# Kernel tuning notes

Hardware: AMD Instinct MI355X
Metric: run time of the kernel (lower is better)

## Reference

```python
import jax, jax.numpy as jnp
import numpy as np

L, D, H, HID, V, MAXLEN = 4, 768, 12, 3072, 32000, 1024
HD = D // H

def _pe_table(max_len, d_model):
    pos = np.arange(max_len)[:, None].astype(np.float64)
    i = np.arange(d_model)[None, :]
    ang = pos / np.power(10000.0, 2 * (i // 2) / d_model)
    ang[:, 0::2] = np.sin(ang[:, 0::2])
    ang[:, 1::2] = np.cos(ang[:, 1::2])
    return jnp.asarray(ang, dtype=jnp.float32)

def _layernorm(x, g, b, eps=1e-5):
    mu = jnp.mean(x, axis=-1, keepdims=True)
    var = jnp.mean(jnp.square(x - mu), axis=-1, keepdims=True)
    return (x - mu) * jax.lax.rsqrt(var + eps) * g + b

def setup_inputs() -> dict:
    key = jax.random.key(0)
    ks = jax.random.split(key, 16)
    s = 0.02
    inp = {
        'tokens': jax.random.randint(ks[0], (4, 1024), 0, V),
        'emb': jax.random.normal(ks[1], (V, D), jnp.float32) * s,
        'pe': _pe_table(MAXLEN, D),
        'ln1_g': jnp.ones((L, D), jnp.float32), 'ln1_b': jnp.zeros((L, D), jnp.float32),
        'wq': jax.random.normal(ks[2], (L, D, D), jnp.float32) * s, 'bq': jnp.zeros((L, D), jnp.float32),
        'wk': jax.random.normal(ks[3], (L, D, D), jnp.float32) * s, 'bk': jnp.zeros((L, D), jnp.float32),
        'wv': jax.random.normal(ks[4], (L, D, D), jnp.float32) * s, 'bv': jnp.zeros((L, D), jnp.float32),
        'wo': jax.random.normal(ks[5], (L, D, D), jnp.float32) * s, 'bo': jnp.zeros((L, D), jnp.float32),
        'ln2_g': jnp.ones((L, D), jnp.float32), 'ln2_b': jnp.zeros((L, D), jnp.float32),
        'w1': jax.random.normal(ks[6], (L, D, HID), jnp.float32) * s, 'b1': jnp.zeros((L, HID), jnp.float32),
        'w2': jax.random.normal(ks[7], (L, HID, D), jnp.float32) * s, 'b2': jnp.zeros((L, D), jnp.float32),
        'lnf_g': jnp.ones((D,), jnp.float32), 'lnf_b': jnp.zeros((D,), jnp.float32),
        'w_out': jax.random.normal(ks[8], (D, V), jnp.float32) * s,
    }
    return inp

def reference(tokens, emb, pe, ln1_g, ln1_b, wq, bq, wk, bk, wv, bv, wo, bo, ln2_g, ln2_b, w1, b1, w2, b2, lnf_g, lnf_b, w_out):
    B, S = tokens.shape
    x = emb[tokens] + pe[:S]  # [B,S,D]
    causal = jnp.tril(jnp.ones((S, S), bool))  # True = keep
    scale = 1.0 / jnp.sqrt(jnp.float32(D))  # NOTE: module scales by sqrt(d_model), not sqrt(head_dim)
    for l in range(L):
        h = _layernorm(x, ln1_g[l], ln1_b[l])
        def heads(w, b):
            return (h @ w + b).reshape(B, S, H, HD).transpose(0, 2, 1, 3)  # [B,H,S,HD]
        q, k, v = heads(wq[l], bq[l]), heads(wk[l], bk[l]), heads(wv[l], bv[l])
        scores = jnp.einsum('bhqd,bhkd->bhqk', q, k) * scale
        scores = jnp.where(causal, scores, -jnp.inf)
        probs = jax.nn.softmax(scores, axis=-1)
        attn = jnp.einsum('bhqk,bhkd->bhqd', probs, v)
        attn = attn.transpose(0, 2, 1, 3).reshape(B, S, D)
        x = x + attn @ wo[l] + bo[l]
        h2 = _layernorm(x, ln2_g[l], ln2_b[l])
        x = x + jax.nn.relu(h2 @ w1[l] + b1[l]) @ w2[l] + b2[l]
    hs = _layernorm(x, lnf_g, lnf_b)
    return hs @ w_out  # [B,S,V]
```

## Files before the change

kernel.cpp:

```cpp
#include <hip/hip_runtime.h>


typedef __bf16 bf16_t;
typedef bf16_t bf16x8 __attribute__((ext_vector_type(8)));
typedef bf16_t bf16x4 __attribute__((ext_vector_type(4)));
typedef float f32x4 __attribute__((ext_vector_type(4)));

#define GLD16(G, L) __builtin_amdgcn_global_load_lds(                          \
    (const __attribute__((address_space(1))) unsigned int*)(const void*)(G),   \
    (__attribute__((address_space(3))) unsigned int*)(void*)(L), 16, 0, 0)

__device__ __forceinline__ f32x4 mfma16(bf16x8 a, bf16x8 b, f32x4 c) {
  return __builtin_amdgcn_mfma_f32_16x16x32_bf16(a, b, c, 0, 0, 0);
}

__device__ __forceinline__ void barrier_raw() {
  asm volatile("s_barrier" ::: "memory");
}

#define RED16_MAX(x) { x = fmaxf(x, __shfl_xor(x, 1)); x = fmaxf(x, __shfl_xor(x, 2)); \
                       x = fmaxf(x, __shfl_xor(x, 4)); x = fmaxf(x, __shfl_xor(x, 8)); }
#define RED16_SUM(x) { x += __shfl_xor(x, 1); x += __shfl_xor(x, 2); \
                       x += __shfl_xor(x, 4); x += __shfl_xor(x, 8); }

__device__ __forceinline__ int SW64(int row, int col) {
  return row * 64 + (col ^ ((row & 7) << 3));
}

__global__ __launch_bounds__(256)
void tconv_k(const float* __restrict__ in, bf16_t* __restrict__ out, int K, int N,
             size_t in_ls, size_t out_ls) {
  __shared__ float tile[32][33];
  in  += (size_t)blockIdx.z * in_ls;
  out += (size_t)blockIdx.z * out_ls;
  const int n0 = blockIdx.x * 32, k0 = blockIdx.y * 32;
  const int tx = threadIdx.x & 31, ty = threadIdx.x >> 5;
#pragma unroll
  for (int j = 0; j < 4; ++j)
    tile[ty + j * 8][tx] = in[(size_t)(k0 + ty + j * 8) * N + n0 + tx];
  __syncthreads();
#pragma unroll
  for (int j = 0; j < 4; ++j)
    out[(size_t)(n0 + ty + j * 8) * K + k0 + tx] = (bf16_t)tile[tx][ty + j * 8];
}

__global__ void qkvbias_k(const float* __restrict__ bq, const float* __restrict__ bk,
                          const float* __restrict__ bv, float* __restrict__ out) {
  const int l = blockIdx.x;
  for (int j = threadIdx.x; j < 2304; j += 256) {
    float v = (j < 768) ? bq[l * 768 + j]
            : (j < 1536) ? bk[l * 768 + j - 768]
                         : bv[l * 768 + j - 1536];
    out[l * 2304 + j] = v;
  }
}

__global__ __launch_bounds__(256)
void embed_k(const int* __restrict__ tok, const float* __restrict__ emb,
             const float* __restrict__ pe, float* __restrict__ xf) {
  const int row = blockIdx.x, tid = threadIdx.x;
  const int s = row & 1023;
  const int t = tok[row];
  float* o = xf + (size_t)row * 768;
  const float* e = emb + (size_t)t * 768;
  const float* p = pe + (size_t)s * 768;
  o[tid]       = e[tid]       + p[tid];
  o[tid + 256] = e[tid + 256] + p[tid + 256];
  o[tid + 512] = e[tid + 512] + p[tid + 512];
}

__global__ __launch_bounds__(256)
void ln_k(const float* __restrict__ x, const float* __restrict__ g,
          const float* __restrict__ bb, bf16_t* __restrict__ out) {
  const int wave = threadIdx.x >> 6, lane = threadIdx.x & 63;
  const int row = blockIdx.x * 4 + wave;
  const float* xr = x + (size_t)row * 768;
  f32x4 v[3];
#pragma unroll
  for (int c = 0; c < 3; ++c) v[c] = *(const f32x4*)&xr[c * 256 + lane * 4];
  float s = 0.0f;
#pragma unroll
  for (int c = 0; c < 3; ++c)
#pragma unroll
    for (int i = 0; i < 4; ++i) s += v[c][i];
#pragma unroll
  for (int off = 32; off; off >>= 1) s += __shfl_xor(s, off);
  const float mu = s * (1.0f / 768.0f);
  float s2 = 0.0f;
#pragma unroll
  for (int c = 0; c < 3; ++c)
#pragma unroll
    for (int i = 0; i < 4; ++i) {
      const float d = v[c][i] - mu;
      s2 += d * d;
    }
#pragma unroll
  for (int off = 32; off; off >>= 1) s2 += __shfl_xor(s2, off);
  const float rstd = rsqrtf(s2 * (1.0f / 768.0f) + 1e-5f);
  bf16_t* orow = out + (size_t)row * 768;
#pragma unroll
  for (int c = 0; c < 3; ++c) {
    const f32x4 gv = *(const f32x4*)&g[c * 256 + lane * 4];
    const f32x4 bv = *(const f32x4*)&bb[c * 256 + lane * 4];
    bf16x4 o;
#pragma unroll
    for (int i = 0; i < 4; ++i)
      o[i] = (bf16_t)((v[c][i] - mu) * rstd * gv[i] + bv[i]);
    *(bf16x4*)&orow[c * 256 + lane * 4] = o;
  }
}

template <bool BIAS, bool RELU, bool OUTF32, bool NT, int SUPER>
__global__ __launch_bounds__(512, 2)
void gemm8p(const bf16_t* __restrict__ A, const bf16_t* __restrict__ BT,
            const float* __restrict__ bias,
            float* __restrict__ outF, bf16_t* __restrict__ outB,
            int M, int N, int K) {
  extern __shared__ char smem[];
  const int NT_TILES = K >> 6;
  const int tilesM = M >> 8;
  const int cpx = gridDim.x >> 3;
  const int blk = ((int)blockIdx.x & 7) * cpx + ((int)blockIdx.x >> 3);
  int tm, tn;
  if (SUPER > 0) {
    const int grp = SUPER * tilesM;
    const int g = blk / grp, r = blk % grp;
    tm = r / SUPER;
    tn = g * SUPER + r % SUPER;
  } else {
    tm = blk % tilesM;
    tn = blk / tilesM;
  }
  const int tid = threadIdx.x;
  const int lane = tid & 63, wave = tid >> 6;
  const int wr = wave >> 2, wc = wave & 3;
  const int lrow = lane & 15, koct = lane >> 4;

  const size_t rowK = (size_t)K * 2;
  const int srow = tid >> 3;
  const int cswz = ((tid & 7) ^ (srow & 7)) << 4;
  const char* gA = (const char*)(A + (size_t)tm * 256 * K) + (size_t)srow * rowK + cswz;
  const char* gB = (const char*)(BT + (size_t)tn * 256 * K) + (size_t)srow * rowK + cswz;

  const int swz = (lrow & 7) << 4;
  const int aB0 = (wr * 128 + lrow) * 128 + ((koct * 16) ^ swz);
  const int bB0 = 32768 + (wc * 64 + lrow) * 128 + ((koct * 16) ^ swz);

  auto stageA = [&](int t) {
    char* d = smem + ((t & 1) << 16);
    const size_t kb = (size_t)t * 128;
    GLD16(gA + kb,              d + tid * 16);
    GLD16(gA + 64 * rowK + kb,  d + 8192 + tid * 16);
    GLD16(gA + 128 * rowK + kb, d + 16384 + tid * 16);
    GLD16(gA + 192 * rowK + kb, d + 24576 + tid * 16);
  };
  auto stageB = [&](int t) {
    char* d = smem + ((t & 1) << 16) + 32768;
    const size_t kb = (size_t)t * 128;
    GLD16(gB + kb,              d + tid * 16);
    GLD16(gB + 64 * rowK + kb,  d + 8192 + tid * 16);
    GLD16(gB + 128 * rowK + kb, d + 16384 + tid * 16);
    GLD16(gB + 192 * rowK + kb, d + 24576 + tid * 16);
  };

  stageA(0); stageB(0);
  stageA(1); stageB(1);

  f32x4 acc[8][4] = {};

  for (int t = 0; t < NT_TILES; ++t) {
    const char* rb = smem + ((t & 1) << 16);
    const bool pf = (t + 2) < NT_TILES;
    if (t == NT_TILES - 1) asm volatile("s_waitcnt vmcnt(0)" ::: "memory");
    else                   asm volatile("s_waitcnt vmcnt(8)" ::: "memory");
    barrier_raw();

    bf16x8 a0[4][2], a1[4][2], b[4][2];
#pragma unroll
    for (int mi = 0; mi < 4; ++mi) {
      const int o = aB0 + mi * 2048;
      a0[mi][0] = *(const bf16x8*)(rb + o);
      a0[mi][1] = *(const bf16x8*)(rb + (o ^ 64));
    }
#pragma unroll
    for (int ni = 0; ni < 2; ++ni) {
      const int o = bB0 + ni * 2048;
      b[ni][0] = *(const bf16x8*)(rb + o);
      b[ni][1] = *(const bf16x8*)(rb + (o ^ 64));
    }
    barrier_raw();
    __builtin_amdgcn_s_setprio(1);
#pragma unroll
    for (int mi = 0; mi < 4; ++mi)
#pragma unroll
      for (int ni = 0; ni < 2; ++ni) {
        acc[mi][ni] = mfma16(a0[mi][0], b[ni][0], acc[mi][ni]);
        acc[mi][ni] = mfma16(a0[mi][1], b[ni][1], acc[mi][ni]);
      }
    __builtin_amdgcn_s_setprio(0);
    barrier_raw();

#pragma unroll
    for (int ni = 2; ni < 4; ++ni) {
      const int o = bB0 + ni * 2048;
      b[ni][0] = *(const bf16x8*)(rb + o);
      b[ni][1] = *(const bf16x8*)(rb + (o ^ 64));
    }
    __builtin_amdgcn_s_setprio(1);
#pragma unroll
    for (int mi = 0; mi < 4; ++mi)
#pragma unroll
      for (int ni = 2; ni < 4; ++ni) {
        acc[mi][ni] = mfma16(a0[mi][0], b[ni][0], acc[mi][ni]);
        acc[mi][ni] = mfma16(a0[mi][1], b[ni][1], acc[mi][ni]);
      }
    __builtin_amdgcn_s_setprio(0);
    asm volatile("s_waitcnt lgkmcnt(0)" ::: "memory");
    barrier_raw();

    if (pf) stageB(t + 2);
#pragma unroll
    for (int mi = 0; mi < 4; ++mi) {
      const int o = aB0 + (mi + 4) * 2048;
      a1[mi][0] = *(const bf16x8*)(rb + o);
      a1[mi][1] = *(const bf16x8*)(rb + (o ^ 64));
    }
    __builtin_amdgcn_s_setprio(1);
#pragma unroll
    for (int mi = 0; mi < 4; ++mi)
#pragma unroll
      for (int ni = 0; ni < 2; ++ni) {
        acc[mi + 4][ni] = mfma16(a1[mi][0], b[ni][0], acc[mi + 4][ni]);
        acc[mi + 4][ni] = mfma16(a1[mi][1], b[ni][1], acc[mi + 4][ni]);
      }
    __builtin_amdgcn_s_setprio(0);
    asm volatile("s_waitcnt lgkmcnt(0)" ::: "memory");
    barrier_raw();

    if (pf) stageA(t + 2);
    __builtin_amdgcn_s_setprio(1);
#pragma unroll
    for (int mi = 0; mi < 4; ++mi)
#pragma unroll
      for (int ni = 2; ni < 4; ++ni) {
        acc[mi + 4][ni] = mfma16(a1[mi][0], b[ni][0], acc[mi + 4][ni]);
        acc[mi + 4][ni] = mfma16(a1[mi][1], b[ni][1], acc[mi + 4][ni]);
      }
    __builtin_amdgcn_s_setprio(0);
  }

  barrier_raw();
  const int row0 = tm * 256 + wr * 128, col0 = tn * 256 + wc * 64;
  float bv[4];
#pragma unroll
  for (int ni = 0; ni < 4; ++ni)
    bv[ni] = BIAS ? bias[col0 + ni * 16 + lrow] : 0.0f;

  if (OUTF32) {
    float* lf = (float*)smem + wave * (32 * 68);
#pragma unroll
    for (int ph = 0; ph < 4; ++ph) {
#pragma unroll
      for (int mm = 0; mm < 2; ++mm) {
        const int mi = ph * 2 + mm;
#pragma unroll
        for (int ni = 0; ni < 4; ++ni)
#pragma unroll
          for (int r = 0; r < 4; ++r) {
            float v = acc[mi][ni][r] + bv[ni];
            if (RELU) v = fmaxf(v, 0.0f);
            lf[(mm * 16 + koct * 4 + r) * 68 + ni * 16 + lrow] = v;
          }
      }
#pragma unroll
      for (int j = 0; j < 8; ++j) {
        const int lr = j * 4 + koct;
        const int lc = lrow * 4;
        f32x4 v4 = *(const f32x4*)&lf[lr * 68 + lc];
        f32x4* dst = (f32x4*)&outF[(size_t)(row0 + ph * 32 + lr) * N + col0 + lc];
        if (NT) __builtin_nontemporal_store(v4, dst);
        else    *dst = v4;
      }
    }
  } else {
    bf16_t* lb = (bf16_t*)smem + wave * (32 * 72);
#pragma unroll
    for (int ph = 0; ph < 4; ++ph) {
#pragma unroll
      for (int mm = 0; mm < 2; ++mm) {
        const int mi = ph * 2 + mm;
#pragma unroll
        for (int ni = 0; ni < 4; ++ni)
#pragma unroll
          for (int r = 0; r < 4; ++r) {
            float v = acc[mi][ni][r] + bv[ni];
            if (RELU) v = fmaxf(v, 0.0f);
            lb[(mm * 16 + koct * 4 + r) * 72 + ni * 16 + lrow] = (bf16_t)v;
          }
      }
#pragma unroll
      for (int j = 0; j < 4; ++j) {
        const int lr = j * 8 + (lane >> 3);
        const int lc = (lane & 7) * 8;
        bf16x8 v8 = *(const bf16x8*)&lb[lr * 72 + lc];
        *(bf16x8*)&outB[(size_t)(row0 + ph * 32 + lr) * N + col0 + lc] = v8;
      }
    }
  }
}

template <bool BIAS, bool RELU>
__global__ __launch_bounds__(512, 4)
void gemm128(const bf16_t* __restrict__ A, const bf16_t* __restrict__ BT,
             const float* __restrict__ bias, bf16_t* __restrict__ outB,
             int M, int N, int K) {
  extern __shared__ char smem[];
  const int NT_TILES = K >> 6;
  const int tilesM = M >> 7;
  const int cpx = gridDim.x >> 3;
  const int blk = ((int)blockIdx.x & 7) * cpx + ((int)blockIdx.x >> 3);
  const int tm = blk % tilesM, tn = blk / tilesM;
  const int tid = threadIdx.x;
  const int lane = tid & 63, wave = tid >> 6;
  const int wr = wave >> 2, wc = wave & 3;
  const int lrow = lane & 15, koct = lane >> 4;

  const size_t rowK = (size_t)K * 2;
  const int srow = tid >> 3;
  const int cswz = ((tid & 7) ^ (srow & 7)) << 4;
  const char* gA = (const char*)(A + (size_t)tm * 128 * K) + (size_t)srow * rowK + cswz;
  const char* gB = (const char*)(BT + (size_t)tn * 128 * K) + (size_t)srow * rowK + cswz;

  const int swz = (lrow & 7) << 4;
  const int aB0 = (wr * 64 + lrow) * 128 + ((koct * 16) ^ swz);
  const int bB0 = 16384 + (wc * 32 + lrow) * 128 + ((koct * 16) ^ swz);

  auto stage = [&](int t) {
    char* d = smem + ((t & 1) << 15);
    const size_t kb = (size_t)t * 128;
    GLD16(gA + kb,             d + tid * 16);
    GLD16(gA + 64 * rowK + kb, d + 8192 + tid * 16);
    GLD16(gB + kb,             d + 16384 + tid * 16);
    GLD16(gB + 64 * rowK + kb, d + 24576 + tid * 16);
  };

  stage(0); stage(1);

  f32x4 acc[4][2] = {};

  for (int t = 0; t < NT_TILES; ++t) {
    const char* rb = smem + ((t & 1) << 15);
    const bool pf = (t + 2) < NT_TILES;
    if (t == NT_TILES - 1) asm volatile("s_waitcnt vmcnt(0)" ::: "memory");
    else                   asm volatile("s_waitcnt vmcnt(4)" ::: "memory");
    barrier_raw();

    bf16x8 a[4], b[2], a2[4], b2[2];
#pragma unroll
    for (int mi = 0; mi < 4; ++mi) a[mi] = *(const bf16x8*)(rb + aB0 + mi * 2048);
#pragma unroll
    for (int ni = 0; ni < 2; ++ni) b[ni] = *(const bf16x8*)(rb + bB0 + ni * 2048);
    barrier_raw();
    __builtin_amdgcn_s_setprio(1);
#pragma unroll
    for (int mi = 0; mi < 4; ++mi)
#pragma unroll
      for (int ni = 0; ni < 2; ++ni)
        acc[mi][ni] = mfma16(a[mi], b[ni], acc[mi][ni]);
    __builtin_amdgcn_s_setprio(0);

#pragma unroll
    for (int mi = 0; mi < 4; ++mi) a2[mi] = *(const bf16x8*)(rb + ((aB0 + mi * 2048) ^ 64));
#pragma unroll
    for (int ni = 0; ni < 2; ++ni) b2[ni] = *(const bf16x8*)(rb + ((bB0 + ni * 2048) ^ 64));
    __builtin_amdgcn_s_setprio(1);
#pragma unroll
    for (int mi = 0; mi < 4; ++mi)
#pragma unroll
      for (int ni = 0; ni < 2; ++ni)
        acc[mi][ni] = mfma16(a2[mi], b2[ni], acc[mi][ni]);
    __builtin_amdgcn_s_setprio(0);
    asm volatile("s_waitcnt lgkmcnt(0)" ::: "memory");
    barrier_raw();
    if (pf) stage(t + 2);
  }

  const int row0 = tm * 128 + wr * 64, col0 = tn * 128 + wc * 32;
  bf16_t* lb = (bf16_t*)smem + wave * (64 * 36);
#pragma unroll
  for (int ni = 0; ni < 2; ++ni) {
    const float bv = BIAS ? bias[col0 + ni * 16 + lrow] : 0.0f;
#pragma unroll
    for (int mi = 0; mi < 4; ++mi)
#pragma unroll
      for (int r = 0; r < 4; ++r) {
        float v = acc[mi][ni][r] + bv;
        if (RELU) v = fmaxf(v, 0.0f);
        lb[(mi * 16 + koct * 4 + r) * 36 + ni * 16 + lrow] = (bf16_t)v;
      }
  }
#pragma unroll
  for (int j = 0; j < 4; ++j) {
    const int lr = j * 16 + (lane >> 2);
    const int lc = (lane & 3) * 8;
    bf16x8 v8 = *(const bf16x8*)&lb[lr * 36 + lc];
    *(bf16x8*)&outB[(size_t)(row0 + lr) * N + col0 + lc] = v8;
  }
}

template <bool BIAS, bool RELU, bool RESID, bool OUTF32>
__global__ __launch_bounds__(256, 2)
void gemmS(const bf16_t* __restrict__ A, const bf16_t* __restrict__ BT,
           const float* __restrict__ bias, const float* __restrict__ resid,
           float* __restrict__ outF, bf16_t* __restrict__ outB,
           int M, int N, int K) {
  extern __shared__ char smem[];
  const int NT = K >> 6;
  const int tiles_n = N >> 7;
  const int tm = blockIdx.x / tiles_n, tn = blockIdx.x % tiles_n;
  const int tid = threadIdx.x;
  const int wave = tid >> 6, lane = tid & 63;
  const int wr = wave >> 1, wc = wave & 1;
  const int lrow = lane & 15, koct = lane >> 4;

  const char* gA[2];
  const char* gB[4];
  {
    const char* Ab = (const char*)(A + (size_t)tm * 64 * K);
    const char* Bb = (const char*)(BT + (size_t)tn * 128 * K);
#pragma unroll
    for (int i = 0; i < 2; ++i) {
      const int off = i * 4096 + tid * 16;
      const int row = off >> 7;
      const int src = off ^ ((row & 7) << 4);
      gA[i] = Ab + (size_t)row * (2 * K) + (src & 127);
    }
#pragma unroll
    for (int i = 0; i < 4; ++i) {
      const int off = i * 4096 + tid * 16;
      const int row = off >> 7;
      const int src = off ^ ((row & 7) << 4);
      gB[i] = Bb + (size_t)row * (2 * K) + (src & 127);
    }
  }

  int aoff[2][2], boff[2][4];
#pragma unroll
  for (int kk = 0; kk < 2; ++kk) {
#pragma unroll
    for (int mi = 0; mi < 2; ++mi) {
      const int row = wr * 32 + mi * 16 + lrow;
      aoff[kk][mi] = (row * 128 + kk * 64 + koct * 16) ^ ((lrow & 7) << 4);
    }
#pragma unroll
    for (int ni = 0; ni < 4; ++ni) {
      const int row = wc * 64 + ni * 16 + lrow;
      boff[kk][ni] = 8192 + ((row * 128 + kk * 64 + koct * 16) ^ ((lrow & 7) << 4));
    }
  }

#pragma unroll
  for (int t = 0; t < 2; ++t) {
    char* sb = smem + t * 24576;
    const size_t kb = (size_t)t * 128;
    GLD16(gA[0] + kb, sb + tid * 16);
    GLD16(gA[1] + kb, sb + 4096 + tid * 16);
    GLD16(gB[0] + kb, sb + 8192 + tid * 16);
    GLD16(gB[1] + kb, sb + 12288 + tid * 16);
    GLD16(gB[2] + kb, sb + 16384 + tid * 16);
    GLD16(gB[3] + kb, sb + 20480 + tid * 16);
  }

  f32x4 acc[2][4] = {};

  for (int t = 0; t < NT; ++t) {
    char* sb = smem + (t % 3) * 24576;
    char* sb2 = smem + ((t + 2) % 3) * 24576;
    const bool pf = (t + 2) < NT;
    const size_t kb2 = (size_t)(t + 2) * 128;

    if (t == NT - 1) asm volatile("s_waitcnt vmcnt(0)" ::: "memory");
    else             asm volatile("s_waitcnt vmcnt(6)" ::: "memory");
    barrier_raw();

#pragma unroll
    for (int kk = 0; kk < 2; ++kk) {
      bf16x8 af[2], bfr[4];
#pragma unroll
      for (int mi = 0; mi < 2; ++mi)
        af[mi] = *(const bf16x8*)(sb + aoff[kk][mi]);
#pragma unroll
      for (int ni = 0; ni < 4; ++ni)
        bfr[ni] = *(const bf16x8*)(sb + boff[kk][ni]);
      if (pf) {
        if (kk == 0) {
          GLD16(gA[0] + kb2, sb2 + tid * 16);
          GLD16(gA[1] + kb2, sb2 + 4096 + tid * 16);
          GLD16(gB[0] + kb2, sb2 + 8192 + tid * 16);
        } else {
          GLD16(gB[1] + kb2, sb2 + 12288 + tid * 16);
          GLD16(gB[2] + kb2, sb2 + 16384 + tid * 16);
          GLD16(gB[3] + kb2, sb2 + 20480 + tid * 16);
        }
      }
      barrier_raw();
      __builtin_amdgcn_s_setprio(1);
#pragma unroll
      for (int mi = 0; mi < 2; ++mi)
#pragma unroll
        for (int ni = 0; ni < 4; ++ni)
          acc[mi][ni] = mfma16(af[mi], bfr[ni], acc[mi][ni]);
      __builtin_amdgcn_s_setprio(0);
    }
  }

  const int row0 = tm * 64 + wr * 32, col0 = tn * 128 + wc * 64;
#pragma unroll
  for (int ni = 0; ni < 4; ++ni) {
    const int col = col0 + ni * 16 + lrow;
    const float bv = BIAS ? bias[col] : 0.0f;
#pragma unroll
    for (int mi = 0; mi < 2; ++mi) {
#pragma unroll
      for (int r = 0; r < 4; ++r) {
        const int row = row0 + mi * 16 + koct * 4 + r;
        float v = acc[mi][ni][r] + bv;
        if (RELU) v = fmaxf(v, 0.0f);
        const size_t idx = (size_t)row * N + col;
        if (RESID) v += resid[idx];
        if (OUTF32) outF[idx] = v;
        else        outB[idx] = (bf16_t)v;
      }
    }
  }
}

__global__ __launch_bounds__(256)
void attn_k(const bf16_t* __restrict__ qkv, bf16_t* __restrict__ ab) {
  __shared__ __align__(16) bf16_t Qs[64 * 64];
  __shared__ __align__(16) bf16_t Ks[64 * 64];
  __shared__ __align__(16) bf16_t Vt[64 * 64];
  __shared__ __align__(16) bf16_t Ps[4][16 * 64];
  const int qt = blockIdx.x, h = blockIdx.y, b = blockIdx.z;
  const int tid = threadIdx.x;
  const int wave = tid >> 6, lane = tid & 63;
  const int lrow = lane & 15, koct = lane >> 4;
  const float scale = 0.03608439182435161f;

  const size_t RS = 2304;
  const bf16_t* qbase = qkv + h * 64;
  const bf16_t* kbase = qkv + 768 + h * 64;
  const bf16_t* vbase = qkv + 1536 + h * 64;

  const int sr = tid >> 3;
  const int sc = (((tid & 7) ^ (sr & 7)) << 3);

  {
#pragma unroll
    for (int i = 0; i < 2; ++i)
      GLD16(qbase + (size_t)(b * 1024 + qt * 64 + i * 32 + sr) * RS + sc,
            Qs + i * 2048 + tid * 8);
  }
  __syncthreads();
  bf16x8 qf[2];
  qf[0] = *(const bf16x8*)&Qs[SW64(wave * 16 + lrow, koct * 8)];
  qf[1] = *(const bf16x8*)&Qs[SW64(wave * 16 + lrow, 32 + koct * 8)];

  float m_r[4], l_r[4];
  f32x4 o[4] = {};
#pragma unroll
  for (int r = 0; r < 4; ++r) { m_r[r] = -1e30f; l_r[r] = 0.0f; }

  for (int kt = 0; kt <= qt; ++kt) {
    __syncthreads();
    {
#pragma unroll
      for (int i = 0; i < 2; ++i)
        GLD16(kbase + (size_t)(b * 1024 + kt * 64 + i * 32 + sr) * RS + sc,
              Ks + i * 2048 + tid * 8);
    }
    {
      const int kvr = lane;
      const int d0 = wave * 16;
      const bf16_t* vr = vbase + (size_t)(b * 1024 + kt * 64 + kvr) * RS + d0;
      bf16x8 v0 = *(const bf16x8*)vr;
      bf16x8 v1 = *(const bf16x8*)(vr + 8);
#pragma unroll
      for (int j = 0; j < 8; ++j) {
        Vt[(d0 + j) * 64 + (kvr ^ (j << 3))]     = v0[j];
        Vt[(d0 + 8 + j) * 64 + (kvr ^ (j << 3))] = v1[j];
      }
    }
    __syncthreads();

    f32x4 s[4] = {};
#pragma unroll
    for (int ni = 0; ni < 4; ++ni) {
      bf16x8 kf0 = *(const bf16x8*)&Ks[SW64(ni * 16 + lrow, koct * 8)];
      bf16x8 kf1 = *(const bf16x8*)&Ks[SW64(ni * 16 + lrow, 32 + koct * 8)];
      s[ni] = mfma16(qf[0], kf0, s[ni]);
      s[ni] = mfma16(qf[1], kf1, s[ni]);
    }

    const int qrow = qt * 64 + wave * 16 + koct * 4;
    float rm[4];
#pragma unroll
    for (int r = 0; r < 4; ++r) rm[r] = -1e30f;
#pragma unroll
    for (int ni = 0; ni < 4; ++ni) {
      const int kcol = kt * 64 + ni * 16 + lrow;
#pragma unroll
      for (int r = 0; r < 4; ++r) {
        float v = s[ni][r] * scale;
        if (kcol > qrow + r) v = -1e30f;
        s[ni][r] = v;
        rm[r] = fmaxf(rm[r], v);
      }
    }
#pragma unroll
    for (int r = 0; r < 4; ++r) RED16_MAX(rm[r]);
    float corr[4], ps[4];
#pragma unroll
    for (int r = 0; r < 4; ++r) {
      const float mn = fmaxf(m_r[r], rm[r]);
      corr[r] = __expf(m_r[r] - mn);
      m_r[r] = mn;
      ps[r] = 0.0f;
    }
#pragma unroll
    for (int ni = 0; ni < 4; ++ni)
#pragma unroll
      for (int r = 0; r < 4; ++r) {
        const float p = __expf(s[ni][r] - m_r[r]);
        s[ni][r] = p;
        ps[r] += p;
      }
#pragma unroll
    for (int r = 0; r < 4; ++r) RED16_SUM(ps[r]);
#pragma unroll
    for (int r = 0; r < 4; ++r) l_r[r] = l_r[r] * corr[r] + ps[r];
#pragma unroll
    for (int ni = 0; ni < 4; ++ni)
#pragma unroll
      for (int r = 0; r < 4; ++r) o[ni][r] *= corr[r];

#pragma unroll
    for (int ni = 0; ni < 4; ++ni)
#pragma unroll
      for (int r = 0; r < 4; ++r) {
        const int prow = koct * 4 + r;
        Ps[wave][prow * 64 + ((ni * 16 + lrow) ^ ((prow & 7) << 3))] =
            (bf16_t)s[ni][r];
      }
    __syncthreads();

    bf16x8 pa0 = *(const bf16x8*)&Ps[wave][SW64(lrow, koct * 8)];
    bf16x8 pa1 = *(const bf16x8*)&Ps[wave][SW64(lrow, 32 + koct * 8)];
#pragma unroll
    for (int ni = 0; ni < 4; ++ni) {
      bf16x8 vf0 = *(const bf16x8*)&Vt[SW64(ni * 16 + lrow, koct * 8)];
      bf16x8 vf1 = *(const bf16x8*)&Vt[SW64(ni * 16 + lrow, 32 + koct * 8)];
      o[ni] = mfma16(pa0, vf0, o[ni]);
      o[ni] = mfma16(pa1, vf1, o[ni]);
    }
  }

#pragma unroll
  for (int r = 0; r < 4; ++r) {
    const float inv = 1.0f / l_r[r];
    const int row = qt * 64 + wave * 16 + koct * 4 + r;
#pragma unroll
    for (int ni = 0; ni < 4; ++ni)
      ab[(size_t)(b * 1024 + row) * 768 + h * 64 + ni * 16 + lrow] =
          (bf16_t)(o[ni][r] * inv);
  }
}

extern "C" void kernel_launch(void* const* d_in, const int* in_sizes, int n_in,
                              void* d_out, int out_size, void* d_ws, size_t ws_size,
                              hipStream_t stream) {
  (void)in_sizes; (void)n_in; (void)out_size; (void)ws_size;
  const int*   tok   = (const int*)d_in[0];
  const float* emb   = (const float*)d_in[1];
  const float* pe    = (const float*)d_in[2];
  const float* ln1_g = (const float*)d_in[3];
  const float* ln1_b = (const float*)d_in[4];
  const float* wq    = (const float*)d_in[5];
  const float* bq    = (const float*)d_in[6];
  const float* wk    = (const float*)d_in[7];
  const float* bk    = (const float*)d_in[8];
  const float* wv    = (const float*)d_in[9];
  const float* bv    = (const float*)d_in[10];
  const float* wo    = (const float*)d_in[11];
  const float* bo    = (const float*)d_in[12];
  const float* ln2_g = (const float*)d_in[13];
  const float* ln2_b = (const float*)d_in[14];
  const float* w1    = (const float*)d_in[15];
  const float* b1    = (const float*)d_in[16];
  const float* w2    = (const float*)d_in[17];
  const float* b2    = (const float*)d_in[18];
  const float* lnf_g = (const float*)d_in[19];
  const float* lnf_b = (const float*)d_in[20];
  const float* w_out = (const float*)d_in[21];
  float* out = (float*)d_out;

  char* ws = (char*)d_ws;
  size_t off = 0;
  auto alloc = [&](size_t bytes) -> void* {
    void* p = ws + off;
    off += (bytes + 255) & ~(size_t)255;
    return p;
  };
  float*  xf      = (float*)alloc(4096ull * 768 * 4);
  bf16_t* hb      = (bf16_t*)alloc(4096ull * 768 * 2);
  bf16_t* qkvb    = (bf16_t*)alloc(4096ull * 2304 * 2);
  bf16_t* ab      = (bf16_t*)alloc(4096ull * 768 * 2);
  bf16_t* fb      = (bf16_t*)alloc(4096ull * 3072 * 2);
  float*  qkvbias = (float*)alloc(4ull * 2304 * 4);
  bf16_t* wqkvT   = (bf16_t*)alloc(4ull * 2304 * 768 * 2);
  bf16_t* woT     = (bf16_t*)alloc(4ull * 768 * 768 * 2);
  bf16_t* w1T     = (bf16_t*)alloc(4ull * 3072 * 768 * 2);
  bf16_t* w2T     = (bf16_t*)alloc(4ull * 768 * 3072 * 2);
  bf16_t* woutT   = (bf16_t*)alloc(32000ull * 768 * 2);

  tconv_k<<<dim3(24, 24, 4), 256, 0, stream>>>(wq, wqkvT, 768, 768,
      768ull * 768, 2304ull * 768);
  tconv_k<<<dim3(24, 24, 4), 256, 0, stream>>>(wk, wqkvT + 768ull * 768, 768, 768,
      768ull * 768, 2304ull * 768);
  tconv_k<<<dim3(24, 24, 4), 256, 0, stream>>>(wv, wqkvT + 2ull * 768 * 768, 768, 768,
      768ull * 768, 2304ull * 768);
  tconv_k<<<dim3(24, 24, 4), 256, 0, stream>>>(wo, woT, 768, 768,
      768ull * 768, 768ull * 768);
  tconv_k<<<dim3(96, 24, 4), 256, 0, stream>>>(w1, w1T, 768, 3072,
      768ull * 3072, 3072ull * 768);
  tconv_k<<<dim3(24, 96, 4), 256, 0, stream>>>(w2, w2T, 3072, 768,
      3072ull * 768, 768ull * 3072);
  tconv_k<<<dim3(1000, 24, 1), 256, 0, stream>>>(w_out, woutT, 768, 32000, 0, 0);
  qkvbias_k<<<4, 256, 0, stream>>>(bq, bk, bv, qkvbias);

  embed_k<<<4096, 256, 0, stream>>>(tok, emb, pe, xf);

  const size_t SMEM8P  = 131072;
  const size_t SMEM128 = 65536;
  const size_t SMEMS   = 3 * 24576;
  for (int l = 0; l < 4; ++l) {
    ln_k<<<1024, 256, 0, stream>>>(xf, ln1_g + l * 768, ln1_b + l * 768, hb);
    gemm128<true, false><<<32 * 18, 512, SMEM128, stream>>>(
        hb, wqkvT + (size_t)l * 2304 * 768, qkvbias + l * 2304,
        qkvb, 4096, 2304, 768);
    attn_k<<<dim3(16, 12, 4), 256, 0, stream>>>(qkvb, ab);
    gemmS<true, false, true, true><<<64 * 6, 256, SMEMS, stream>>>(
        ab, woT + (size_t)l * 768 * 768, bo + l * 768,
        xf, xf, nullptr, 4096, 768, 768);
    ln_k<<<1024, 256, 0, stream>>>(xf, ln2_g + l * 768, ln2_b + l * 768, hb);
    gemm128<true, true><<<32 * 24, 512, SMEM128, stream>>>(
        hb, w1T + (size_t)l * 3072 * 768, b1 + l * 3072,
        fb, 4096, 3072, 768);
    gemmS<true, false, true, true><<<64 * 6, 256, SMEMS, stream>>>(
        fb, w2T + (size_t)l * 768 * 3072, b2 + l * 768,
        xf, xf, nullptr, 4096, 768, 3072);
  }
  ln_k<<<1024, 256, 0, stream>>>(xf, lnf_g, lnf_b, hb);
  gemm8p<false, false, true, true, 5><<<16 * 125, 512, SMEM8P, stream>>>(
      hb, woutT, nullptr, out, nullptr, 4096, 32000, 768);
}
```

Measured before the change: 1.048 ms.

## Add 256-thread 128x128 GEMM kernel and rebalance GEMM kernels across layers

Adds a new gemmV kernel: 128x128 tiles, 4 waves each computing a 64x64 sub-tile, BK=32 double-buffered with global_load_lds, 32 KB shared memory and up to 4 blocks per CU. It replaces gemm128 for the FFN up-projection and gemm8p for the vocabulary projection. The QKV projection moves to the large 256-row gemm8p tile. The aim is better occupancy and per-wave register reuse on the largest GEMMs. The trade-off is shorter K steps per barrier, and a different grid size and tail balance per GEMM.

```diff
diff --git a/kernel.cpp b/kernel.cpp
--- a/kernel.cpp
+++ b/kernel.cpp
@@ -107,6 +107,144 @@
     for (int i = 0; i < 4; ++i)
       o[i] = (bf16_t)((v[c][i] - mu) * rstd * gv[i] + bv[i]);
     *(bf16x4*)&orow[c * 256 + lane * 4] = o;
+  }
+}
+
+template <bool BIAS, bool RELU, bool OUTF32, bool NT, int SUPER>
+__global__ __launch_bounds__(256, 4)
+void gemmV(const bf16_t* __restrict__ A, const bf16_t* __restrict__ BT,
+           const float* __restrict__ bias,
+           float* __restrict__ outF, bf16_t* __restrict__ outB,
+           int M, int N, int K) {
+  extern __shared__ char smem[];
+  const int NT_TILES = K >> 5;
+  const int tilesM = M >> 7;
+  const int cpx = gridDim.x >> 3;
+  const int blk = ((int)blockIdx.x & 7) * cpx + ((int)blockIdx.x >> 3);
+  int tm, tn;
+  if (SUPER > 0) {
+    const int grp = SUPER * tilesM;
+    const int g = blk / grp, r = blk % grp;
+    tm = r / SUPER;
+    tn = g * SUPER + r % SUPER;
+  } else {
+    tm = blk % tilesM;
+    tn = blk / tilesM;
+  }
+  const int tid = threadIdx.x;
+  const int lane = tid & 63, wave = tid >> 6;
+  const int wr = wave >> 1, wc = wave & 1;
+  const int lrow = lane & 15, koct = lane >> 4;
+
+  const size_t rowK = (size_t)K * 2;
+  const int srow = tid >> 2;
+  const int cswz = ((tid & 3) ^ ((tid >> 3) & 3)) << 4;
+  const char* gA = (const char*)(A + (size_t)tm * 128 * K) + (size_t)srow * rowK + cswz;
+  const char* gB = (const char*)(BT + (size_t)tn * 128 * K) + (size_t)srow * rowK + cswz;
+
+  const int fkey = (lrow >> 1) & 3;
+  const int aB0 = (wr * 64 + lrow) * 64 + ((koct ^ fkey) << 4);
+  const int bB0 = 8192 + (wc * 64 + lrow) * 64 + ((koct ^ fkey) << 4);
+
+  auto stage = [&](int t) {
+    char* d = smem + ((t & 1) << 14);
+    const size_t kb = (size_t)t * 64;
+    GLD16(gA + kb,             d + tid * 16);
+    GLD16(gA + 64 * rowK + kb, d + 4096 + tid * 16);
+    GLD16(gB + kb,             d + 8192 + tid * 16);
+    GLD16(gB + 64 * rowK + kb, d + 12288 + tid * 16);
+  };
+
+  stage(0); stage(1);
+
+  f32x4 acc[4][4] = {};
+
+  for (int t = 0; t < NT_TILES; ++t) {
+    const char* rb = smem + ((t & 1) << 14);
+    const bool pf = (t + 2) < NT_TILES;
+    if (t == NT_TILES - 1) asm volatile("s_waitcnt vmcnt(0)" ::: "memory");
+    else                   asm volatile("s_waitcnt vmcnt(4)" ::: "memory");
+    barrier_raw();
+
+    bf16x8 a[4], b[4];
+#pragma unroll
+    for (int mi = 0; mi < 4; ++mi) a[mi] = *(const bf16x8*)(rb + aB0 + mi * 1024);
+#pragma unroll
+    for (int ni = 0; ni < 2; ++ni) b[ni] = *(const bf16x8*)(rb + bB0 + ni * 1024);
+    barrier_raw();
+    __builtin_amdgcn_s_setprio(1);
+#pragma unroll
+    for (int mi = 0; mi < 4; ++mi)
+#pragma unroll
+      for (int ni = 0; ni < 2; ++ni)
+        acc[mi][ni] = mfma16(a[mi], b[ni], acc[mi][ni]);
+    __builtin_amdgcn_s_setprio(0);
+
+#pragma unroll
+    for (int ni = 2; ni < 4; ++ni) b[ni] = *(const bf16x8*)(rb + bB0 + ni * 1024);
+    __builtin_amdgcn_s_setprio(1);
+#pragma unroll
+    for (int mi = 0; mi < 4; ++mi)
+#pragma unroll
+      for (int ni = 2; ni < 4; ++ni)
+        acc[mi][ni] = mfma16(a[mi], b[ni], acc[mi][ni]);
+    __builtin_amdgcn_s_setprio(0);
+    asm volatile("s_waitcnt lgkmcnt(0)" ::: "memory");
+    barrier_raw();
+    if (pf) stage(t + 2);
+  }
+
+  const int row0 = tm * 128 + wr * 64, col0 = tn * 128 + wc * 64;
+  float bv[4];
+#pragma unroll
+  for (int ni = 0; ni < 4; ++ni)
+    bv[ni] = BIAS ? bias[col0 + ni * 16 + lrow] : 0.0f;
+
+  if (OUTF32) {
+    float* lf = (float*)(smem + wave * 8192);
+#pragma unroll
+    for (int p = 0; p < 2; ++p) {
+#pragma unroll
+      for (int mm = 0; mm < 2; ++mm) {
+        const int mi = p * 2 + mm;
+#pragma unroll
+        for (int ni = 0; ni < 4; ++ni)
+#pragma unroll
+          for (int r = 0; r < 4; ++r) {
+            float v = acc[mi][ni][r] + bv[ni];
+            if (RELU) v = fmaxf(v, 0.0f);
+            lf[(mm * 16 + koct * 4 + r) * 64 + ni * 16 + lrow] = v;
+          }
+      }
+#pragma unroll
+      for (int j = 0; j < 8; ++j) {
+        const int lr = j * 4 + koct;
+        const int lc = lrow * 4;
+        f32x4 v4 = *(const f32x4*)&lf[lr * 64 + lc];
+        f32x4* dst = (f32x4*)&outF[(size_t)(row0 + p * 32 + lr) * N + col0 + lc];
+        if (NT) __builtin_nontemporal_store(v4, dst);
+        else    *dst = v4;
+      }
+    }
+  } else {
+    bf16_t* lb = (bf16_t*)(smem + wave * 8192);
+#pragma unroll
+    for (int mi = 0; mi < 4; ++mi)
+#pragma unroll
+      for (int ni = 0; ni < 4; ++ni)
+#pragma unroll
+        for (int r = 0; r < 4; ++r) {
+          float v = acc[mi][ni][r] + bv[ni];
+          if (RELU) v = fmaxf(v, 0.0f);
+          lb[(mi * 16 + koct * 4 + r) * 64 + ni * 16 + lrow] = (bf16_t)v;
+        }
+#pragma unroll
+    for (int j = 0; j < 8; ++j) {
+      const int lr = j * 8 + (lane >> 3);
+      const int lc = (lane & 7) * 8;
+      bf16x8 v8 = *(const bf16x8*)&lb[lr * 64 + lc];
+      *(bf16x8*)&outB[(size_t)(row0 + lr) * N + col0 + lc] = v8;
+    }
   }
 }
 
@@ -306,105 +444,6 @@
         *(bf16x8*)&outB[(size_t)(row0 + ph * 32 + lr) * N + col0 + lc] = v8;
       }
     }
-  }
-}
-
-template <bool BIAS, bool RELU>
-__global__ __launch_bounds__(512, 4)
-void gemm128(const bf16_t* __restrict__ A, const bf16_t* __restrict__ BT,
-             const float* __restrict__ bias, bf16_t* __restrict__ outB,
-             int M, int N, int K) {
-  extern __shared__ char smem[];
-  const int NT_TILES = K >> 6;
-  const int tilesM = M >> 7;
-  const int cpx = gridDim.x >> 3;
-  const int blk = ((int)blockIdx.x & 7) * cpx + ((int)blockIdx.x >> 3);
-  const int tm = blk % tilesM, tn = blk / tilesM;
-  const int tid = threadIdx.x;
-  const int lane = tid & 63, wave = tid >> 6;
-  const int wr = wave >> 2, wc = wave & 3;
-  const int lrow = lane & 15, koct = lane >> 4;
-
-  const size_t rowK = (size_t)K * 2;
-  const int srow = tid >> 3;
-  const int cswz = ((tid & 7) ^ (srow & 7)) << 4;
-  const char* gA = (const char*)(A + (size_t)tm * 128 * K) + (size_t)srow * rowK + cswz;
-  const char* gB = (const char*)(BT + (size_t)tn * 128 * K) + (size_t)srow * rowK + cswz;
-
-  const int swz = (lrow & 7) << 4;
-  const int aB0 = (wr * 64 + lrow) * 128 + ((koct * 16) ^ swz);
-  const int bB0 = 16384 + (wc * 32 + lrow) * 128 + ((koct * 16) ^ swz);
-
-  auto stage = [&](int t) {
-    char* d = smem + ((t & 1) << 15);
-    const size_t kb = (size_t)t * 128;
-    GLD16(gA + kb,             d + tid * 16);
-    GLD16(gA + 64 * rowK + kb, d + 8192 + tid * 16);
-    GLD16(gB + kb,             d + 16384 + tid * 16);
-    GLD16(gB + 64 * rowK + kb, d + 24576 + tid * 16);
-  };
-
-  stage(0); stage(1);
-
-  f32x4 acc[4][2] = {};
-
-  for (int t = 0; t < NT_TILES; ++t) {
-    const char* rb = smem + ((t & 1) << 15);
-    const bool pf = (t + 2) < NT_TILES;
-    if (t == NT_TILES - 1) asm volatile("s_waitcnt vmcnt(0)" ::: "memory");
-    else                   asm volatile("s_waitcnt vmcnt(4)" ::: "memory");
-    barrier_raw();
-
-    bf16x8 a[4], b[2], a2[4], b2[2];
-#pragma unroll
-    for (int mi = 0; mi < 4; ++mi) a[mi] = *(const bf16x8*)(rb + aB0 + mi * 2048);
-#pragma unroll
-    for (int ni = 0; ni < 2; ++ni) b[ni] = *(const bf16x8*)(rb + bB0 + ni * 2048);
-    barrier_raw();
-    __builtin_amdgcn_s_setprio(1);
-#pragma unroll
-    for (int mi = 0; mi < 4; ++mi)
-#pragma unroll
-      for (int ni = 0; ni < 2; ++ni)
-        acc[mi][ni] = mfma16(a[mi], b[ni], acc[mi][ni]);
-    __builtin_amdgcn_s_setprio(0);
-
-#pragma unroll
-    for (int mi = 0; mi < 4; ++mi) a2[mi] = *(const bf16x8*)(rb + ((aB0 + mi * 2048) ^ 64));
-#pragma unroll
-    for (int ni = 0; ni < 2; ++ni) b2[ni] = *(const bf16x8*)(rb + ((bB0 + ni * 2048) ^ 64));
-    __builtin_amdgcn_s_setprio(1);
-#pragma unroll
-    for (int mi = 0; mi < 4; ++mi)
-#pragma unroll
-      for (int ni = 0; ni < 2; ++ni)
-        acc[mi][ni] = mfma16(a2[mi], b2[ni], acc[mi][ni]);
-    __builtin_amdgcn_s_setprio(0);
-    asm volatile("s_waitcnt lgkmcnt(0)" ::: "memory");
-    barrier_raw();
-    if (pf) stage(t + 2);
-  }
-
-  const int row0 = tm * 128 + wr * 64, col0 = tn * 128 + wc * 32;
-  bf16_t* lb = (bf16_t*)smem + wave * (64 * 36);
-#pragma unroll
-  for (int ni = 0; ni < 2; ++ni) {
-    const float bv = BIAS ? bias[col0 + ni * 16 + lrow] : 0.0f;
-#pragma unroll
-    for (int mi = 0; mi < 4; ++mi)
-#pragma unroll
-      for (int r = 0; r < 4; ++r) {
-        float v = acc[mi][ni][r] + bv;
-        if (RELU) v = fmaxf(v, 0.0f);
-        lb[(mi * 16 + koct * 4 + r) * 36 + ni * 16 + lrow] = (bf16_t)v;
-      }
-  }
-#pragma unroll
-  for (int j = 0; j < 4; ++j) {
-    const int lr = j * 16 + (lane >> 2);
-    const int lc = (lane & 3) * 8;
-    bf16x8 v8 = *(const bf16x8*)&lb[lr * 36 + lc];
-    *(bf16x8*)&outB[(size_t)(row0 + lr) * N + col0 + lc] = v8;
   }
 }
 
@@ -740,27 +779,27 @@
 
   embed_k<<<4096, 256, 0, stream>>>(tok, emb, pe, xf);
 
-  const size_t SMEM8P  = 131072;
-  const size_t SMEM128 = 65536;
-  const size_t SMEMS   = 3 * 24576;
+  const size_t SMEM8P = 131072;
+  const size_t SMEMV  = 32768;
+  const size_t SMEMS  = 3 * 24576;
   for (int l = 0; l < 4; ++l) {
     ln_k<<<1024, 256, 0, stream>>>(xf, ln1_g + l * 768, ln1_b + l * 768, hb);
-    gemm128<true, false><<<32 * 18, 512, SMEM128, stream>>>(
+    gemm8p<true, false, false, false, 0><<<16 * 9, 512, SMEM8P, stream>>>(
         hb, wqkvT + (size_t)l * 2304 * 768, qkvbias + l * 2304,
-        qkvb, 4096, 2304, 768);
+        nullptr, qkvb, 4096, 2304, 768);
     attn_k<<<dim3(16, 12, 4), 256, 0, stream>>>(qkvb, ab);
     gemmS<true, false, true, true><<<64 * 6, 256, SMEMS, stream>>>(
         ab, woT + (size_t)l * 768 * 768, bo + l * 768,
         xf, xf, nullptr, 4096, 768, 768);
     ln_k<<<1024, 256, 0, stream>>>(xf, ln2_g + l * 768, ln2_b + l * 768, hb);
-    gemm128<true, true><<<32 * 24, 512, SMEM128, stream>>>(
+    gemmV<true, true, false, false, 0><<<32 * 24, 256, SMEMV, stream>>>(
         hb, w1T + (size_t)l * 3072 * 768, b1 + l * 3072,
-        fb, 4096, 3072, 768);
+        nullptr, fb, 4096, 3072, 768);
     gemmS<true, false, true, true><<<64 * 6, 256, SMEMS, stream>>>(
         fb, w2T + (size_t)l * 768 * 3072, b2 + l * 768,
         xf, xf, nullptr, 4096, 768, 3072);
   }
   ln_k<<<1024, 256, 0, stream>>>(xf, lnf_g, lnf_b, hb);
-  gemm8p<false, false, true, true, 5><<<16 * 125, 512, SMEM8P, stream>>>(
+  gemmV<false, false, true, true, 10><<<32 * 250, 256, SMEMV, stream>>>(
       hb, woutT, nullptr, out, nullptr, 4096, 32000, 768);
 }
```

Result: faster. 1.024 ms (-2.3%).
